# Performance work log

Hardware: AMD Instinct MI355X
Metric: run time of the kernel (lower is better)

## Reference

```python
import jax, jax.numpy as jnp
import numpy as np
from jax.scipy.special import logsumexp

NEG = -1e30  # stand-in for -inf that is safe under fp32 and vjp
MAX_SEG_LEN = 64
WITH_TRANSITION = True


def setup_inputs() -> dict:
    key = jax.random.key(0)
    k1, k2 = jax.random.split(key)
    B, S, L = 8, 512, 32
    segment_score = jax.random.normal(k1, (B, S, S, L), dtype=jnp.float32)
    transitions = jax.random.uniform(k2, (L, L), dtype=jnp.float32)  # matches nn.init.uniform_(0,1)
    return {"segment_score": segment_score, "transitions": transitions}


def _compute_log_z(segment_score, transitions, max_seg_len=MAX_SEG_LEN, with_transition=WITH_TRANSITION):
    # segment_score: [B, S, S, L] (start, end, label); transitions: [L, L]
    B, S, _, L = segment_score.shape
    M = max_seg_len
    dt = segment_score.dtype
    diag = jnp.diagonal(transitions)  # [L]

    # alpha_pad slot (p + M) holds log_alpha at frame p; slots < M act as -inf guard
    alpha_pad = jnp.full((B, S + M, L), NEG, dtype=dt)
    alpha_pad = alpha_pad.at[:, M, :].set(segment_score[:, 0, 0, :])

    w = jnp.arange(M)
    j = (M - w).astype(dt)  # window slot w corresponds to segment length j = M - w
    # transition term for a continuation segment of length j ending in label cur, coming from prev:
    # T[prev, cur] + diag[cur] * (j - 1)   -> [M, prev, cur]
    trans_term = transitions[None, :, :] + diag[None, None, :] * (j[:, None, None] - 1.0)

    def step(alpha_pad, f_end):
        # segment scores for all segments ending at f_end: [B, S, L]
        seg_col = jax.lax.dynamic_index_in_dim(segment_score, f_end, axis=2, keepdims=False)
        # pad so window slot w maps to start position f_end - M + 1 + w (length j = M - w)
        seg_pad = jnp.pad(seg_col, ((0, 0), (M - 1, 0), (0, 0)))
        seg_win = jax.lax.dynamic_slice_in_dim(seg_pad, f_end, M, axis=1)     # [B, M, L]
        # alpha window slot w -> frame f_end - M + w = f_end - j (guarded by NEG padding)
        alpha_win = jax.lax.dynamic_slice_in_dim(alpha_pad, f_end, M, axis=1)  # [B, M, L]

        # continuation scores: alpha[prev] + seg * j (+ transition)  -> [B, M, prev, cur]
        scores = alpha_win[:, :, :, None] + (seg_win * j[None, :, None])[:, :, None, :]
        if with_transition:
            scores = scores + trans_term[None, :, :, :]

        # initial segment [0, f_end] (no predecessor), only valid while f_end + 1 <= M
        f = f_end.astype(dt)
        init = seg_col[:, 0, :] * (f + 1.0)
        if with_transition:
            init = init + diag[None, :] * f
        init = jnp.where(f_end < M, init, NEG)

        all_scores = jnp.concatenate([scores.reshape(B, M * L, L), init[:, None, :]], axis=1)
        new_alpha = logsumexp(all_scores, axis=1)  # [B, L]

        alpha_pad = jax.lax.dynamic_update_slice_in_dim(
            alpha_pad, new_alpha[:, None, :], f_end + M, axis=1)
        return alpha_pad, None

    alpha_pad, _ = jax.lax.scan(step, alpha_pad, jnp.arange(1, S))
    log_z = logsumexp(alpha_pad[:, S - 1 + M, :], axis=1)  # [B]
    return log_z


def reference(segment_score, transitions):
    return _compute_log_z(segment_score, transitions)
```

## Files before the change

kernel.cpp:

```cpp
#include <hip/hip_runtime.h>

#define NEGF (-1e30f)

constexpr int S = 512;
constexpr int L = 32;


template <int CTRL>
__device__ __forceinline__ float dppf(float x) {
    return __builtin_bit_cast(float,
        __builtin_amdgcn_update_dpp(0, __builtin_bit_cast(int, x),
                                    CTRL, 0xf, 0xf, true));
}
#define GR8_MAX(v) do { v = fmaxf(v, dppf<0xB1>(v));    \
                        v = fmaxf(v, dppf<0x4E>(v));    \
                        v = fmaxf(v, dppf<0x141>(v)); } while (0)
#define GR8_ADD(v) do { v += dppf<0xB1>(v);                                 \
                        v += dppf<0x4E>(v);                                 \
                        v += dppf<0x141>(v); } while (0)

#define LDS_BARRIER() do {                                                  \
    __builtin_amdgcn_fence(__ATOMIC_RELEASE, "workgroup", "local");         \
    __builtin_amdgcn_s_barrier();                                           \
    __builtin_amdgcn_fence(__ATOMIC_ACQUIRE, "workgroup", "local");         \
} while (0)

#define PREFETCH(dst, fe_) do {                                             \
    int fe2 = (fe_); if (fe2 > S - 1) fe2 = S - 1;                          \
    _Pragma("unroll")                                                       \
    for (int i = 0; i < 8; ++i) {                                           \
        const int j0 = jg * 8 + i + 1;                                      \
        int st = fe2 - j0 + 1; st = st < 0 ? 0 : st;                        \
        dst[i] = segB[((size_t)st * S + fe2) * L];                          \
    }                                                                       \
} while (0)

#define PHASE2(p_) do {                                                     \
    const int p_v = (p_);                                                   \
    const float4 a4 = *(const float4*)&alpha[p_v & 1][jg * 4];              \
    float mx = fmaxf(fmaxf(a4.x, a4.y), fmaxf(a4.z, a4.w));                 \
    GR8_MAX(mx);                                                            \
    float sb = __expf(a4.x - mx) * E0 + __expf(a4.y - mx) * E1              \
             + __expf(a4.z - mx) * E2 + __expf(a4.w - mx) * E3;             \
    GR8_ADD(sb);                                                            \
    if (jg == 0) ring[(p_v & 63) * 33 + cur] = mx + __logf(sb);             \
} while (0)

#define STEP(fe_, sv, EARLY) do {                                           \
    const int fe_v = (fe_);                                                 \
    float term[8];                                                          \
    _Pragma("unroll")                                                       \
    for (int i = 0; i < 8; ++i) {                                           \
        const int j0 = jg * 8 + i + 1;                                      \
        const float base = fmaf(sv[i], (float)j0, diag_c * (float)(j0 - 1));\
        float tv;                                                           \
        if (EARLY) {                                                        \
            tv = NEGF;                                                      \
            if (j0 <= fe_v)          tv = ring[((fe_v - j0) & 63) * 33 + cur] + base; \
            else if (j0 == fe_v + 1) tv = base;                             \
        } else {                                                            \
            tv = ring[((fe_v - j0) & 63) * 33 + cur] + base;                \
        }                                                                   \
        term[i] = tv;                                                       \
    }                                                                       \
    float M = fmaxf(fmaxf(fmaxf(term[0], term[1]), fmaxf(term[2], term[3])),\
                    fmaxf(fmaxf(term[4], term[5]), fmaxf(term[6], term[7])));\
    GR8_MAX(M);                                                             \
    float ss = ((__expf(term[0] - M) + __expf(term[1] - M)) +               \
                (__expf(term[2] - M) + __expf(term[3] - M))) +              \
               ((__expf(term[4] - M) + __expf(term[5] - M)) +               \
                (__expf(term[6] - M) + __expf(term[7] - M)));               \
    GR8_ADD(ss);                                                            \
    if (jg == 0) alpha[fe_v & 1][cur] = M + __logf(ss);                     \
    LDS_BARRIER();                                                          \
    PHASE2(fe_v);                                                           \
} while (0)

__launch_bounds__(256, 1)
__global__ void semicrf_fwd(const float* __restrict__ seg,
                            const float* __restrict__ trans,
                            float* __restrict__ out)
{
    const int t   = threadIdx.x;
    const int b   = blockIdx.x;
    const int cur = t >> 3;
    const int jg  = t & 7;

    __shared__ float ring[64 * 33];
    __shared__ float alpha[2][32];

    const float diag_c = trans[cur * 33];
    const float E0 = __expf(trans[(jg * 4 + 0) * 32 + cur]);
    const float E1 = __expf(trans[(jg * 4 + 1) * 32 + cur]);
    const float E2 = __expf(trans[(jg * 4 + 2) * 32 + cur]);
    const float E3 = __expf(trans[(jg * 4 + 3) * 32 + cur]);

    if (t < 32)
        alpha[0][t] = seg[(size_t)b * S * S * L + t];
    __syncthreads();
    PHASE2(0);

    const float* segB = seg + (size_t)b * S * S * L + cur;

    float sv0[8], sv1[8], sv2[8], sv3[8];
    PREFETCH(sv0, 1);
    PREFETCH(sv1, 2);

    for (int fe = 1; fe <= 61; fe += 4) {
        PREFETCH(sv2, fe + 2); STEP(fe + 0, sv0, true);
        PREFETCH(sv3, fe + 3); STEP(fe + 1, sv1, true);
        PREFETCH(sv0, fe + 4); STEP(fe + 2, sv2, true);
        PREFETCH(sv1, fe + 5); STEP(fe + 3, sv3, true);
    }
    for (int fe = 65; fe <= 505; fe += 4) {
        PREFETCH(sv2, fe + 2); STEP(fe + 0, sv0, false);
        PREFETCH(sv3, fe + 3); STEP(fe + 1, sv1, false);
        PREFETCH(sv0, fe + 4); STEP(fe + 2, sv2, false);
        PREFETCH(sv1, fe + 5); STEP(fe + 3, sv3, false);
    }
    PREFETCH(sv2, 511);
    STEP(509, sv0, false);
    STEP(510, sv1, false);
    STEP(511, sv2, false);

    if (t < 64) {
        float v  = (t < 32) ? alpha[1][t] : NEGF;
        float m  = v;
        float ss = 1.f;
        #pragma unroll
        for (int mk = 1; mk <= 32; mk <<= 1) {
            const float m2 = __shfl_xor(m, mk);
            const float s2 = __shfl_xor(ss, mk);
            const float mn = fmaxf(m, m2);
            ss = ss * __expf(m - mn) + s2 * __expf(m2 - mn);
            m  = mn;
        }
        if (t == 0) out[b] = m + __logf(ss);
    }
}

extern "C" void kernel_launch(void* const* d_in, const int* in_sizes, int n_in,
                              void* d_out, int out_size, void* d_ws, size_t ws_size,
                              hipStream_t stream) {
    const float* seg   = (const float*)d_in[0];
    const float* trans = (const float*)d_in[1];
    float* out = (float*)d_out;
    hipLaunchKernelGGL(semicrf_fwd, dim3(8), dim3(256), 0, stream,
                       seg, trans, out);
}
```

Before: 695.1 us.

## Split each step into lead j=1 term and lagged partial logsumexp to cut critical path

Restructures the recurrence so that the partial logsumexp over segment lengths j>=2 is computed one step ahead, off the critical path. The serial dependency then only needs the j=1 term combined with a precomputed (max,sum) pair. Alpha is passed as (max,sum) pairs instead of log values, which removes a log from each step. Per-step work on the dependency chain shrinks, in exchange for more complex indexing, extra state registers and a sentinel row in the ring buffer.

```diff
diff --git a/kernel.cpp b/kernel.cpp
--- a/kernel.cpp
+++ b/kernel.cpp
@@ -25,56 +25,83 @@
     __builtin_amdgcn_fence(__ATOMIC_ACQUIRE, "workgroup", "local");         \
 } while (0)
 
-#define PREFETCH(dst, fe_) do {                                             \
-    int fe2 = (fe_); if (fe2 > S - 1) fe2 = S - 1;                          \
+#define PF_LAG(dst, f_) do {                                                \
+    int fe2 = (f_); if (fe2 > S - 1) fe2 = S - 1;                           \
     _Pragma("unroll")                                                       \
     for (int i = 0; i < 8; ++i) {                                           \
-        const int j0 = jg * 8 + i + 1;                                      \
+        const int j0 = jg * 8 + i + 2;                                      \
         int st = fe2 - j0 + 1; st = st < 0 ? 0 : st;                        \
         dst[i] = segB[((size_t)st * S + fe2) * L];                          \
     }                                                                       \
 } while (0)
 
-#define PHASE2(p_) do {                                                     \
-    const int p_v = (p_);                                                   \
-    const float4 a4 = *(const float4*)&alpha[p_v & 1][jg * 4];              \
-    float mx = fmaxf(fmaxf(a4.x, a4.y), fmaxf(a4.z, a4.w));                 \
-    GR8_MAX(mx);                                                            \
-    float sb = __expf(a4.x - mx) * E0 + __expf(a4.y - mx) * E1              \
-             + __expf(a4.z - mx) * E2 + __expf(a4.w - mx) * E3;             \
-    GR8_ADD(sb);                                                            \
-    if (jg == 0) ring[(p_v & 63) * 33 + cur] = mx + __logf(sb);             \
-} while (0)
-
-#define STEP(fe_, sv, EARLY) do {                                           \
-    const int fe_v = (fe_);                                                 \
-    float term[8];                                                          \
+#define PF_S1(dst, f_) do {                                                 \
+    int fe2 = (f_); if (fe2 > S - 1) fe2 = S - 1;                           \
+    dst = segB[(size_t)fe2 * (S + 1) * L];                                  \
+} while (0)
+
+#define LAGLOAD(f_, lim_, rr) do {                                          \
+    const int f_v = (f_); const int lim_v = (lim_);                         \
     _Pragma("unroll")                                                       \
     for (int i = 0; i < 8; ++i) {                                           \
-        const int j0 = jg * 8 + i + 1;                                      \
-        const float base = fmaf(sv[i], (float)j0, diag_c * (float)(j0 - 1));\
-        float tv;                                                           \
-        if (EARLY) {                                                        \
-            tv = NEGF;                                                      \
-            if (j0 <= fe_v)          tv = ring[((fe_v - j0) & 63) * 33 + cur] + base; \
-            else if (j0 == fe_v + 1) tv = base;                             \
-        } else {                                                            \
-            tv = ring[((fe_v - j0) & 63) * 33 + cur] + base;                \
-        }                                                                   \
-        term[i] = tv;                                                       \
+        const int j0 = jg * 8 + i + 2;                                      \
+        int row = (f_v - j0) & 63;                                          \
+        if (j0 > lim_v || (i == 0 && jg == 0)) row = 64;                    \
+        rr[i] = ring[row * 33 + cur];                                       \
     }                                                                       \
-    float M = fmaxf(fmaxf(fmaxf(term[0], term[1]), fmaxf(term[2], term[3])),\
-                    fmaxf(fmaxf(term[4], term[5]), fmaxf(term[6], term[7])));\
+} while (0)
+
+#define LEAD(k_, s1v_) do {                                                 \
+    const float t1m = bm + (s1v_);                                          \
+    const float Ma  = fmaxf(pM, t1m);                                       \
+    const float Sa  = pS * __expf(pM - Ma) + __expf(t1m - Ma);              \
+    if (jg == 0) {                                                          \
+        *(float2*)&aMS[(k_)&1][cur * 2] = make_float2(Ma, Sa);              \
+        ring[(((k_) - 1) & 63) * 33 + cur] = bm;                            \
+    }                                                                       \
+} while (0)
+
+#define LAGCOMP(sv, rr) do {                                                \
+    float tt[8];                                                            \
+    _Pragma("unroll")                                                       \
+    for (int i = 0; i < 8; ++i)                                             \
+        tt[i] = rr[i] + fmaf(sv[i], jf[i], dj[i]);                          \
+    if (jg == 0) tt[0] = bm + fmaf(sv[0], jf[0], dj[0]);                    \
+    float M = fmaxf(fmaxf(fmaxf(tt[0],tt[1]), fmaxf(tt[2],tt[3])),          \
+                    fmaxf(fmaxf(tt[4],tt[5]), fmaxf(tt[6],tt[7])));         \
     GR8_MAX(M);                                                             \
-    float ss = ((__expf(term[0] - M) + __expf(term[1] - M)) +               \
-                (__expf(term[2] - M) + __expf(term[3] - M))) +              \
-               ((__expf(term[4] - M) + __expf(term[5] - M)) +               \
-                (__expf(term[6] - M) + __expf(term[7] - M)));               \
-    GR8_ADD(ss);                                                            \
-    if (jg == 0) alpha[fe_v & 1][cur] = M + __logf(ss);                     \
+    float SS = ((__expf(tt[0]-M) + __expf(tt[1]-M)) +                       \
+                (__expf(tt[2]-M) + __expf(tt[3]-M))) +                      \
+               ((__expf(tt[4]-M) + __expf(tt[5]-M)) +                       \
+                (__expf(tt[6]-M) + __expf(tt[7]-M)));                       \
+    GR8_ADD(SS);                                                            \
+    pM = M; pS = SS;                                                        \
+} while (0)
+
+#define PHASE2(k_) do {                                                     \
+    const int par = (k_) & 1;                                               \
+    const float4 A0 = *(const float4*)&aMS[par][jg * 8];                    \
+    const float4 A1 = *(const float4*)&aMS[par][jg * 8 + 4];                \
+    float mx = fmaxf(fmaxf(A0.x, A0.z), fmaxf(A1.x, A1.z));                 \
+    GR8_MAX(mx);                                                            \
+    float sb = (A0.y * E0) * __expf(A0.x - mx) +                            \
+               (A0.w * E1) * __expf(A0.z - mx) +                            \
+               (A1.y * E2) * __expf(A1.x - mx) +                            \
+               (A1.w * E3) * __expf(A1.z - mx);                             \
+    GR8_ADD(sb);                                                            \
+    bm = mx + __logf(sb);                                                   \
+} while (0)
+
+#define STEP(k_, sv, s1v_, lim_) do {                                       \
+    float rr[8];                                                            \
+    LAGLOAD((k_) + 1, lim_, rr);                                            \
+    LEAD(k_, s1v_);                                                         \
     LDS_BARRIER();                                                          \
-    PHASE2(fe_v);                                                           \
-} while (0)
+    LAGCOMP(sv, rr);                                                        \
+    PHASE2(k_);                                                             \
+} while (0)
+
+#define LIMV(kk) (((kk) + 2) < 64 ? ((kk) + 2) : 64)
 
 __launch_bounds__(256, 1)
 __global__ void semicrf_fwd(const float* __restrict__ seg,
@@ -86,8 +113,8 @@
     const int cur = t >> 3;
     const int jg  = t & 7;
 
-    __shared__ float ring[64 * 33];
-    __shared__ float alpha[2][32];
+    __shared__ float ring[65 * 33];
+    __shared__ __align__(16) float aMS[2][64];
 
     const float diag_c = trans[cur * 33];
     const float E0 = __expf(trans[(jg * 4 + 0) * 32 + cur]);
@@ -95,36 +122,67 @@
     const float E2 = __expf(trans[(jg * 4 + 2) * 32 + cur]);
     const float E3 = __expf(trans[(jg * 4 + 3) * 32 + cur]);
 
-    if (t < 32)
-        alpha[0][t] = seg[(size_t)b * S * S * L + t];
+    float jf[8], dj[8];
+    #pragma unroll
+    for (int i = 0; i < 8; ++i) {
+        const int j0 = jg * 8 + i + 2;
+        jf[i] = (float)j0;
+        dj[i] = diag_c * (float)(j0 - 1);
+    }
+
+    const float* segB = seg + (size_t)b * S * S * L + cur;
+
+    float sv0[8], sv1[8], sv2[8], sv3[8];
+    float s10, s11, s12, s13;
+    PF_LAG(sv1, 1); PF_LAG(sv2, 2); PF_LAG(sv3, 3); PF_LAG(sv0, 4);
+    PF_S1(s11, 1);  PF_S1(s12, 2);  PF_S1(s13, 3);  PF_S1(s10, 4);
+
+    if (t < 32) {
+        ring[63 * 33 + t] = 0.0f;
+        ring[64 * 33 + t] = NEGF;
+    }
+    if (jg == 0) {
+        const float a0 = segB[0];
+        *(float2*)&aMS[0][cur * 2] = make_float2(a0, 1.0f);
+    }
     __syncthreads();
-    PHASE2(0);
-
-    const float* segB = seg + (size_t)b * S * S * L + cur;
-
-    float sv0[8], sv1[8], sv2[8], sv3[8];
-    PREFETCH(sv0, 1);
-    PREFETCH(sv1, 2);
-
-    for (int fe = 1; fe <= 61; fe += 4) {
-        PREFETCH(sv2, fe + 2); STEP(fe + 0, sv0, true);
-        PREFETCH(sv3, fe + 3); STEP(fe + 1, sv1, true);
-        PREFETCH(sv0, fe + 4); STEP(fe + 2, sv2, true);
-        PREFETCH(sv1, fe + 5); STEP(fe + 3, sv3, true);
-    }
-    for (int fe = 65; fe <= 505; fe += 4) {
-        PREFETCH(sv2, fe + 2); STEP(fe + 0, sv0, false);
-        PREFETCH(sv3, fe + 3); STEP(fe + 1, sv1, false);
-        PREFETCH(sv0, fe + 4); STEP(fe + 2, sv2, false);
-        PREFETCH(sv1, fe + 5); STEP(fe + 3, sv3, false);
-    }
-    PREFETCH(sv2, 511);
-    STEP(509, sv0, false);
-    STEP(510, sv1, false);
-    STEP(511, sv2, false);
+
+    float pM = NEGF, pS = 0.0f, bm = 0.0f;
+
+    {
+        float rr[8];
+        LAGLOAD(1, 2, rr);
+        LDS_BARRIER();
+        LAGCOMP(sv1, rr);
+        PHASE2(0);
+    }
+    PF_LAG(sv1, 5);
+
+    for (int k = 1; k <= 61; k += 4) {
+        STEP(k + 0, sv2, s11, LIMV(k + 0)); PF_LAG(sv2, k + 5); PF_S1(s11, k + 4);
+        STEP(k + 1, sv3, s12, LIMV(k + 1)); PF_LAG(sv3, k + 6); PF_S1(s12, k + 5);
+        STEP(k + 2, sv0, s13, LIMV(k + 2)); PF_LAG(sv0, k + 7); PF_S1(s13, k + 6);
+        STEP(k + 3, sv1, s10, LIMV(k + 3)); PF_LAG(sv1, k + 8); PF_S1(s10, k + 7);
+    }
+    for (int k = 65; k <= 505; k += 4) {
+        STEP(k + 0, sv2, s11, 64); PF_LAG(sv2, k + 5); PF_S1(s11, k + 4);
+        STEP(k + 1, sv3, s12, 64); PF_LAG(sv3, k + 6); PF_S1(s12, k + 5);
+        STEP(k + 2, sv0, s13, 64); PF_LAG(sv0, k + 7); PF_S1(s13, k + 6);
+        STEP(k + 3, sv1, s10, 64); PF_LAG(sv1, k + 8); PF_S1(s10, k + 7);
+    }
+    STEP(509, sv2, s11, 64);
+    STEP(510, sv3, s12, 64);
+
+    {
+        const float t1m = bm + s13;
+        const float Ma  = fmaxf(pM, t1m);
+        const float Sa  = pS * __expf(pM - Ma) + __expf(t1m - Ma);
+        if (jg == 0) *(float2*)&aMS[1][cur * 2] = make_float2(Ma, Sa);
+    }
+    __syncthreads();
 
     if (t < 64) {
-        float v  = (t < 32) ? alpha[1][t] : NEGF;
+        float v  = (t < 32) ? (aMS[1][t * 2] + __logf(aMS[1][t * 2 + 1])) : NEGF;
         float m  = v;
         float ss = 1.f;
         #pragma unroll
```

Measured after the change: 664.9 us. 1.05x faster.

## Split semi-CRF recurrence into critical-chain wave and lagged partial-sum waves

Applied to the files above, without the earlier changes.

Restructures the sequential forward pass. One wavefront now computes only the latency-critical short-lag terms (lengths 1-3) plus the transition matmul. Three other wavefronts precompute logsumexp partials for segment lengths 4-64 a few frames ahead and hand them over through LDS, synchronising with spin-wait counters instead of block-wide barriers. The aim is to shorten the per-frame critical path and remove the s_barrier each frame. In exchange the code relies on volatile-counter producer/consumer ordering, which carries correctness and deadlock risk.

```diff
diff --git a/kernel.cpp b/kernel.cpp
--- a/kernel.cpp
+++ b/kernel.cpp
@@ -12,130 +12,225 @@
         __builtin_amdgcn_update_dpp(0, __builtin_bit_cast(int, x),
                                     CTRL, 0xf, 0xf, true));
 }
-#define GR8_MAX(v) do { v = fmaxf(v, dppf<0xB1>(v));    \
-                        v = fmaxf(v, dppf<0x4E>(v));    \
-                        v = fmaxf(v, dppf<0x141>(v)); } while (0)
-#define GR8_ADD(v) do { v += dppf<0xB1>(v);                                 \
-                        v += dppf<0x4E>(v);                                 \
-                        v += dppf<0x141>(v); } while (0)
-
-#define LDS_BARRIER() do {                                                  \
-    __builtin_amdgcn_fence(__ATOMIC_RELEASE, "workgroup", "local");         \
-    __builtin_amdgcn_s_barrier();                                           \
+#define RED32_MAX(v) do { v = fmaxf(v, dppf<0xB1>(v));                      \
+                          v = fmaxf(v, dppf<0x4E>(v));                      \
+                          v = fmaxf(v, dppf<0x141>(v));                     \
+                          v = fmaxf(v, dppf<0x140>(v));                     \
+                          v = fmaxf(v, __shfl_xor(v, 16)); } while (0)
+#define RED32_ADD(v) do { v += dppf<0xB1>(v); v += dppf<0x4E>(v);           \
+                          v += dppf<0x141>(v); v += dppf<0x140>(v);         \
+                          v += __shfl_xor(v, 16); } while (0)
+
+template<int JLO, int NT0, int NT1, int W>
+__device__ __forceinline__ void lag_run(const float* __restrict__ segB,
+                                        const float* __restrict__ trans,
+                                        float* ring,
+                                        float (*part)[3][32][2],
+                                        volatile int* cnt,
+                                        int c, int h, bool lane0)
+{
+    const float diag_c = trans[c * 33];
+    const int nt = h ? NT1 : NT0;
+    const int jb = JLO + (h ? NT0 : 0);
+    float jfv[11], djv[11];
+    int idxA[11], idxB[11];
+#pragma unroll
+    for (int i = 0; i < 11; ++i) {
+        const int jj = (i < nt) ? (jb + i) : jb;
+        jfv[i] = (float)jj;
+        djv[i] = diag_c * (float)(jj - 1);
+        idxA[i] = (3 * (S + 1) - (jj - 1) * S) * L + c;
+        idxB[i] = idxA[i] + (S + 1) * L;
+    }
+    float svA[11], svB[11];
+    int cd = -1;
+
+#define LAG_PF(sv, idx, fq, MSK) do {                                       \
+    _Pragma("unroll")                                                       \
+    for (int i = 0; i < 11; ++i) {                                          \
+        int e = idx[i];                                                     \
+        if (MSK) {                                                          \
+            const bool vld = (i < nt) && (jb + i <= (fq) + 1);              \
+            e = vld ? e : ((fq) * L + c);      \
+        }                                                                   \
+        sv[i] = segB[e];                                                    \
+        idx[i] += 2 * (S + 1) * L;           \
+    }                                                                       \
+} while (0)
+
+#define LAG_FRAME(f_, sv, MSK) do {                                         \
+    const int ff = (f_);                                                    \
+    if (cd < ff - 4) {                                                      \
+        do { __builtin_amdgcn_s_sleep(1); cd = cnt[3]; } while (cd < ff - 4); \
+    }                                                                       \
     __builtin_amdgcn_fence(__ATOMIC_ACQUIRE, "workgroup", "local");         \
+    const int fj = ff - jb;                                                 \
+    float tt[11];                                                           \
+    _Pragma("unroll")                                                       \
+    for (int i = 0; i < 11; ++i) {                                          \
+        const float rv = ring[((fj - i) & 63) * 33 + c];                    \
+        const float tv = rv + fmaf(sv[i], jfv[i], djv[i]);                  \
+        bool vld = (i < nt);                                                \
+        if (MSK) vld = vld && (jb + i <= ff + 1);                           \
+        tt[i] = vld ? tv : NEGF;                                            \
+    }                                                                       \
+    float m = fmaxf(fmaxf(fmaxf(fmaxf(tt[0], tt[1]), fmaxf(tt[2], tt[3])),  \
+                          fmaxf(fmaxf(tt[4], tt[5]), fmaxf(tt[6], tt[7]))), \
+                    fmaxf(fmaxf(tt[8], tt[9]), tt[10]));                    \
+    float s = ((__expf(tt[0] - m) + __expf(tt[1] - m)) +                    \
+               (__expf(tt[2] - m) + __expf(tt[3] - m))) +                   \
+              ((__expf(tt[4] - m) + __expf(tt[5] - m)) +                    \
+               (__expf(tt[6] - m) + __expf(tt[7] - m))) +                   \
+              ((__expf(tt[8] - m) + __expf(tt[9] - m)) +                    \
+               __expf(tt[10] - m));                                         \
+    const float m2 = __shfl_xor(m, 32);                                     \
+    const float s2 = __shfl_xor(s, 32);                                     \
+    const float Mw = fmaxf(m, m2);                                          \
+    const float Sw = s * __expf(m - Mw) + s2 * __expf(m2 - Mw);             \
+    if (h == 0) *(float2*)&part[ff & 3][W][c][0] = make_float2(Mw, Sw);     \
+    asm volatile("s_waitcnt lgkmcnt(0)" ::: "memory");                      \
+    if (lane0) cnt[W] = ff;                                                 \
 } while (0)
 
-#define PREFETCH(dst, fe_) do {                                             \
-    int fe2 = (fe_); if (fe2 > S - 1) fe2 = S - 1;                          \
-    _Pragma("unroll")                                                       \
-    for (int i = 0; i < 8; ++i) {                                           \
-        const int j0 = jg * 8 + i + 1;                                      \
-        int st = fe2 - j0 + 1; st = st < 0 ? 0 : st;                        \
-        dst[i] = segB[((size_t)st * S + fe2) * L];                          \
-    }                                                                       \
-} while (0)
-
-#define PHASE2(p_) do {                                                     \
-    const int p_v = (p_);                                                   \
-    const float4 a4 = *(const float4*)&alpha[p_v & 1][jg * 4];              \
-    float mx = fmaxf(fmaxf(a4.x, a4.y), fmaxf(a4.z, a4.w));                 \
-    GR8_MAX(mx);                                                            \
-    float sb = __expf(a4.x - mx) * E0 + __expf(a4.y - mx) * E1              \
-             + __expf(a4.z - mx) * E2 + __expf(a4.w - mx) * E3;             \
-    GR8_ADD(sb);                                                            \
-    if (jg == 0) ring[(p_v & 63) * 33 + cur] = mx + __logf(sb);             \
-} while (0)
-
-#define STEP(fe_, sv, EARLY) do {                                           \
-    const int fe_v = (fe_);                                                 \
-    float term[8];                                                          \
-    _Pragma("unroll")                                                       \
-    for (int i = 0; i < 8; ++i) {                                           \
-        const int j0 = jg * 8 + i + 1;                                      \
-        const float base = fmaf(sv[i], (float)j0, diag_c * (float)(j0 - 1));\
-        float tv;                                                           \
-        if (EARLY) {                                                        \
-            tv = NEGF;                                                      \
-            if (j0 <= fe_v)          tv = ring[((fe_v - j0) & 63) * 33 + cur] + base; \
-            else if (j0 == fe_v + 1) tv = base;                             \
-        } else {                                                            \
-            tv = ring[((fe_v - j0) & 63) * 33 + cur] + base;                \
-        }                                                                   \
-        term[i] = tv;                                                       \
-    }                                                                       \
-    float M = fmaxf(fmaxf(fmaxf(term[0], term[1]), fmaxf(term[2], term[3])),\
-                    fmaxf(fmaxf(term[4], term[5]), fmaxf(term[6], term[7])));\
-    GR8_MAX(M);                                                             \
-    float ss = ((__expf(term[0] - M) + __expf(term[1] - M)) +               \
-                (__expf(term[2] - M) + __expf(term[3] - M))) +              \
-               ((__expf(term[4] - M) + __expf(term[5] - M)) +               \
-                (__expf(term[6] - M) + __expf(term[7] - M)));               \
-    GR8_ADD(ss);                                                            \
-    if (jg == 0) alpha[fe_v & 1][cur] = M + __logf(ss);                     \
-    LDS_BARRIER();                                                          \
-    PHASE2(fe_v);                                                           \
-} while (0)
+    LAG_PF(svA, idxA, 3, true);
+    LAG_PF(svB, idxB, 4, true);
+    for (int f = 3; f <= 61; f += 2) {
+        LAG_FRAME(f, svA, true);      LAG_PF(svA, idxA, f + 2, true);
+        LAG_FRAME(f + 1, svB, true);  LAG_PF(svB, idxB, f + 3, true);
+    }
+    for (int f = 63; f <= 507; f += 2) {
+        LAG_FRAME(f, svA, false);     LAG_PF(svA, idxA, f + 2, false);
+        LAG_FRAME(f + 1, svB, false); LAG_PF(svB, idxB, f + 3, false);
+    }
+    LAG_FRAME(509, svA, false);
+    LAG_PF(svA, idxA, 511, false);
+    LAG_FRAME(510, svB, false);
+    LAG_FRAME(511, svA, false);
+#undef LAG_PF
+#undef LAG_FRAME
+}
 
 __launch_bounds__(256, 1)
 __global__ void semicrf_fwd(const float* __restrict__ seg,
                             const float* __restrict__ trans,
                             float* __restrict__ out)
 {
-    const int t   = threadIdx.x;
-    const int b   = blockIdx.x;
-    const int cur = t >> 3;
-    const int jg  = t & 7;
+    const int t  = threadIdx.x;
+    const int b  = blockIdx.x;
+    const int c  = t & 31;
+    const int h  = (t >> 5) & 1;
+    const int wv = t >> 6;
 
     __shared__ float ring[64 * 33];
-    __shared__ float alpha[2][32];
-
-    const float diag_c = trans[cur * 33];
-    const float E0 = __expf(trans[(jg * 4 + 0) * 32 + cur]);
-    const float E1 = __expf(trans[(jg * 4 + 1) * 32 + cur]);
-    const float E2 = __expf(trans[(jg * 4 + 2) * 32 + cur]);
-    const float E3 = __expf(trans[(jg * 4 + 3) * 32 + cur]);
-
-    if (t < 32)
-        alpha[0][t] = seg[(size_t)b * S * S * L + t];
+    __shared__ __align__(16) float part[4][3][32][2];
+    __shared__ __align__(16) float ubuf[32];
+    __shared__ int cnt_s[4];
+
+    for (int i = t; i < 4 * 3 * 32; i += 256)
+        ((float2*)part)[i] = make_float2(NEGF, 0.f);
+    if (t < 32) ring[63 * 33 + t] = 0.f;
+    if (t < 3)  cnt_s[t] = 2;
+    if (t == 3) cnt_s[3] = -1;
     __syncthreads();
-    PHASE2(0);
-
-    const float* segB = seg + (size_t)b * S * S * L + cur;
-
-    float sv0[8], sv1[8], sv2[8], sv3[8];
-    PREFETCH(sv0, 1);
-    PREFETCH(sv1, 2);
-
-    for (int fe = 1; fe <= 61; fe += 4) {
-        PREFETCH(sv2, fe + 2); STEP(fe + 0, sv0, true);
-        PREFETCH(sv3, fe + 3); STEP(fe + 1, sv1, true);
-        PREFETCH(sv0, fe + 4); STEP(fe + 2, sv2, true);
-        PREFETCH(sv1, fe + 5); STEP(fe + 3, sv3, true);
-    }
-    for (int fe = 65; fe <= 505; fe += 4) {
-        PREFETCH(sv2, fe + 2); STEP(fe + 0, sv0, false);
-        PREFETCH(sv3, fe + 3); STEP(fe + 1, sv1, false);
-        PREFETCH(sv0, fe + 4); STEP(fe + 2, sv2, false);
-        PREFETCH(sv1, fe + 5); STEP(fe + 3, sv3, false);
-    }
-    PREFETCH(sv2, 511);
-    STEP(509, sv0, false);
-    STEP(510, sv1, false);
-    STEP(511, sv2, false);
-
-    if (t < 64) {
-        float v  = (t < 32) ? alpha[1][t] : NEGF;
-        float m  = v;
-        float ss = 1.f;
-        #pragma unroll
-        for (int mk = 1; mk <= 32; mk <<= 1) {
-            const float m2 = __shfl_xor(m, mk);
-            const float s2 = __shfl_xor(ss, mk);
-            const float mn = fmaxf(m, m2);
-            ss = ss * __expf(m - mn) + s2 * __expf(m2 - mn);
-            m  = mn;
+
+    const float* segB  = seg + (size_t)b * S * S * L;
+    volatile int* cnt  = cnt_s;
+
+    if (wv == 0) {
+        __builtin_amdgcn_s_setprio(1);
+        float E[16];
+#pragma unroll
+        for (int i = 0; i < 16; ++i)
+            E[i] = __expf(trans[(h * 16 + i) * 32 + c]);
+        const float diag_c = trans[c * 33];
+
+        float s1s[4], s2s[4], s3s[4];
+#pragma unroll
+        for (int ff = 1; ff <= 4; ++ff) {
+            const int st1 = ff, st2 = ff - 1, st3 = (ff - 2 < 0) ? 0 : ff - 2;
+            s1s[ff & 3] = segB[(st1 * S + ff) * L + c];
+            s2s[ff & 3] = segB[(st2 * S + ff) * L + c];
+            s3s[ff & 3] = segB[(st3 * S + ff) * L + c];
         }
-        if (t == 0) out[b] = m + __logf(ss);
+
+        float Ma = segB[c];
+        float Sa = 1.f;
+        float bm1 = 0.f;
+        float bm2 = NEGF;
+        int lmin = 2, l0 = 2, l1 = 2, l2 = 2;
+
+#define CHAIN_FRAME(f_, Q_) do {                                            \
+    const int ff = (f_);                                                    \
+    if (lmin < ff + 1) {                                                    \
+        do { l0 = cnt[0]; l1 = cnt[1]; l2 = cnt[2];                         \
+             lmin = min(min(l0, l1), l2); } while (lmin < ff + 1);          \
+    }                                                                       \
+    __builtin_amdgcn_fence(__ATOMIC_ACQUIRE, "workgroup", "local");         \
+                                         \
+    float mx = Ma;                                                          \
+    RED32_MAX(mx);                                                          \
+    const float uu = Sa * __expf(Ma - mx);                                  \
+    if (h == 0) ubuf[c] = uu;                                               \
+    if (t == 0) cnt[3] = ff - 1;    \
+    asm volatile("s_waitcnt lgkmcnt(0)" ::: "memory");                      \
+    const float4 uA = *(const float4*)&ubuf[h * 16 + 0];                    \
+    const float4 uB = *(const float4*)&ubuf[h * 16 + 4];                    \
+    const float4 uC = *(const float4*)&ubuf[h * 16 + 8];                    \
+    const float4 uD = *(const float4*)&ubuf[h * 16 + 12];                   \
+    const float2 P0 = *(const float2*)&part[Q_][0][c][0];                   \
+    const float2 P1 = *(const float2*)&part[Q_][1][c][0];                   \
+    const float2 P2 = *(const float2*)&part[Q_][2][c][0];                   \
+    l0 = cnt[0]; l1 = cnt[1]; l2 = cnt[2];                                  \
+    float dA = fmaf(uA.x, E[0],  fmaf(uA.y, E[1],  fmaf(uA.z, E[2],  uA.w * E[3])));  \
+    float dB = fmaf(uB.x, E[4],  fmaf(uB.y, E[5],  fmaf(uB.z, E[6],  uB.w * E[7])));  \
+    float dC = fmaf(uC.x, E[8],  fmaf(uC.y, E[9],  fmaf(uC.z, E[10], uC.w * E[11]))); \
+    float dD = fmaf(uD.x, E[12], fmaf(uD.y, E[13], fmaf(uD.z, E[14], uD.w * E[15]))); \
+    float dot = (dA + dB) + (dC + dD);                                      \
+    dot += __shfl_xor(dot, 32);                                             \
+    const float bb = mx + __logf(dot);                                      \
+    if (h == 0) ring[(ff & 63) * 33 + c] = bb;                              \
+                    \
+    const float t2v = fmaf(2.f, s2s[Q_], bm1 + diag_c);                     \
+    const float t3v = fmaf(3.f, s3s[Q_], bm2 + 2.f * diag_c);               \
+    const float Mp  = fmaxf(fmaxf(P0.x, P1.x), fmaxf(P2.x, fmaxf(t2v, t3v)));        \
+    const float Sp  = P0.y * __expf(P0.x - Mp) + P1.y * __expf(P1.x - Mp)            \
+                    + P2.y * __expf(P2.x - Mp)                              \
+                    + __expf(t2v - Mp) + __expf(t3v - Mp);                  \
+    const float t1v = bb + s1s[Q_];                                         \
+    Ma = fmaxf(Mp, t1v);                                                    \
+    Sa = fmaf(Sp, __expf(Mp - Ma), __expf(t1v - Ma));                       \
+    bm2 = bm1; bm1 = bb;                                                    \
+    lmin = min(min(l0, l1), l2);                                            \
+    { int fq = ff + 5; if (fq > 511) fq = 511;                              \
+      const int bidx = fq * (S + 1) * L + c;                                \
+      s1s[Q_] = segB[bidx];                                                 \
+      s2s[Q_] = segB[bidx - S * L];                                         \
+      s3s[Q_] = segB[bidx - 2 * S * L]; }                                   \
+} while (0)
+
+        for (int fb = 0; fb < 508; fb += 4) {
+            CHAIN_FRAME(fb + 0, 1);
+            CHAIN_FRAME(fb + 1, 2);
+            CHAIN_FRAME(fb + 2, 3);
+            CHAIN_FRAME(fb + 3, 0);
+        }
+        CHAIN_FRAME(508, 1);
+        CHAIN_FRAME(509, 2);
+        CHAIN_FRAME(510, 3);
+#undef CHAIN_FRAME
+        {
+            float mx = Ma;
+            RED32_MAX(mx);
+            float uu = Sa * __expf(Ma - mx);
+            RED32_ADD(uu);
+            if (t == 0) out[b] = mx + __logf(uu);
+        }
+    } else if (wv == 1) {
+        lag_run<4, 11, 10, 0>(segB, trans, ring, part, cnt, c, h, (t & 63) == 0);
+    } else if (wv == 2) {
+        lag_run<25, 10, 10, 1>(segB, trans, ring, part, cnt, c, h, (t & 63) == 0);
+    } else {
+        lag_run<45, 10, 10, 2>(segB, trans, ring, part, cnt, c, h, (t & 63) == 0);
     }
 }
 
```

New measurement: 789.5 us. 1.14x slower.

## Split semi-CRF recurrence into latency-critical chain wave and lagged producer waves

Applied to the files above, without the earlier changes.

The kernel is restructured into one wavefront that runs the serial recurrence with only the short-lag terms (segment lengths 1-15), plus three producer wavefronts. The producers precompute partial logsumexp contributions for the long-lag terms (lengths 16-64) several frames ahead and hand them over through LDS, synchronising with spin-polled counters instead of block barriers. The transition step becomes an exp-space dot product over a broadcast buffer. This aims to shorten the per-frame critical path and remove the workgroup barrier from every step. In exchange it adds custom spin-wait synchronisation with a capped spin count, which risks races or silent wrong results if the lag assumptions are off.

```diff
diff --git a/kernel.cpp b/kernel.cpp
--- a/kernel.cpp
+++ b/kernel.cpp
@@ -4,6 +4,13 @@
 
 constexpr int S = 512;
 constexpr int L = 32;
+constexpr int SL1 = (S + 1) * L;
+constexpr int SLN = S * L;
+constexpr int SSL = S * S * L;
+constexpr int RSTR = 33;
+constexpr int RROWS = 128;
+constexpr int RWRAP = RROWS * RSTR;
+constexpr int SPIN_CAP = 1 << 20;
 
 
 template <int CTRL>
@@ -12,68 +19,130 @@
         __builtin_amdgcn_update_dpp(0, __builtin_bit_cast(int, x),
                                     CTRL, 0xf, 0xf, true));
 }
-#define GR8_MAX(v) do { v = fmaxf(v, dppf<0xB1>(v));    \
-                        v = fmaxf(v, dppf<0x4E>(v));    \
-                        v = fmaxf(v, dppf<0x141>(v)); } while (0)
-#define GR8_ADD(v) do { v += dppf<0xB1>(v);                                 \
-                        v += dppf<0x4E>(v);                                 \
-                        v += dppf<0x141>(v); } while (0)
-
-#define LDS_BARRIER() do {                                                  \
-    __builtin_amdgcn_fence(__ATOMIC_RELEASE, "workgroup", "local");         \
-    __builtin_amdgcn_s_barrier();                                           \
-    __builtin_amdgcn_fence(__ATOMIC_ACQUIRE, "workgroup", "local");         \
+#define RED32_MAX(v) do { v = fmaxf(v, dppf<0xB1>(v));                      \
+                          v = fmaxf(v, dppf<0x4E>(v));                      \
+                          v = fmaxf(v, dppf<0x141>(v));                     \
+                          v = fmaxf(v, dppf<0x140>(v));                     \
+                          v = fmaxf(v, __shfl_xor(v, 16)); } while (0)
+
+#define CHAIN(ff_, SBUF, DOPOLL, DOPUB) do {                                \
+    const int ff = (ff_);                                                   \
+       \
+    float tj[14];                                                           \
+    _Pragma("unroll")                                                       \
+    for (int i = 0; i < 14; ++i)                                            \
+        tj[i] = bH[i] + fmaf(SBUF[i + 1], (float)(i + 2), dgc[i]);          \
+    float Mp = fmaxf(pp1.x, tj[0]);                                         \
+    _Pragma("unroll")                                                       \
+    for (int i = 1; i < 14; ++i) Mp = fmaxf(Mp, tj[i]);                     \
+    float Sp = pp1.y * __expf(pp1.x - Mp);                                  \
+    _Pragma("unroll")                                                       \
+    for (int i = 0; i < 14; ++i) Sp += __expf(tj[i] - Mp);                  \
+    float mxn = Ma;                                                         \
+    RED32_MAX(mxn);                     \
+                               \
+    const float uu = Sa * __expf(Ma - mx);                                  \
+    if (t < 32) ubuf[c] = uu;                                               \
+    const float4 u0 = *(const float4*)&ubuf[0];                             \
+    const float4 u1 = *(const float4*)&ubuf[4];                             \
+    const float4 u2 = *(const float4*)&ubuf[8];                             \
+    const float4 u3 = *(const float4*)&ubuf[12];                            \
+    const float4 u4 = *(const float4*)&ubuf[16];                            \
+    const float4 u5 = *(const float4*)&ubuf[20];                            \
+    const float4 u6 = *(const float4*)&ubuf[24];                            \
+    const float4 u7 = *(const float4*)&ubuf[28];                            \
+    float d0 = u0.x * E[0];                                                 \
+    d0 = fmaf(u0.y, E[1], d0);  d0 = fmaf(u0.z, E[2], d0);                  \
+    d0 = fmaf(u0.w, E[3], d0);  d0 = fmaf(u1.x, E[4], d0);                  \
+    d0 = fmaf(u1.y, E[5], d0);  d0 = fmaf(u1.z, E[6], d0);                  \
+    d0 = fmaf(u1.w, E[7], d0);                                              \
+    float d1 = u2.x * E[8];                                                 \
+    d1 = fmaf(u2.y, E[9],  d1); d1 = fmaf(u2.z, E[10], d1);                 \
+    d1 = fmaf(u2.w, E[11], d1); d1 = fmaf(u3.x, E[12], d1);                 \
+    d1 = fmaf(u3.y, E[13], d1); d1 = fmaf(u3.z, E[14], d1);                 \
+    d1 = fmaf(u3.w, E[15], d1);                                             \
+    float d2 = u4.x * E[16];                                                \
+    d2 = fmaf(u4.y, E[17], d2); d2 = fmaf(u4.z, E[18], d2);                 \
+    d2 = fmaf(u4.w, E[19], d2); d2 = fmaf(u5.x, E[20], d2);                 \
+    d2 = fmaf(u5.y, E[21], d2); d2 = fmaf(u5.z, E[22], d2);                 \
+    d2 = fmaf(u5.w, E[23], d2);                                             \
+    float d3 = u6.x * E[24];                                                \
+    d3 = fmaf(u6.y, E[25], d3); d3 = fmaf(u6.z, E[26], d3);                 \
+    d3 = fmaf(u6.w, E[27], d3); d3 = fmaf(u7.x, E[28], d3);                 \
+    d3 = fmaf(u7.y, E[29], d3); d3 = fmaf(u7.z, E[30], d3);                 \
+    d3 = fmaf(u7.w, E[31], d3);                                             \
+    const float dot = (d0 + d1) + (d2 + d3);                                \
+    const float bb = mx + __logf(dot);                                      \
+    if (t < 32) ring[wadr] = bb;                                            \
+    wadr += RSTR; if (wadr >= RWRAP) wadr -= RWRAP;                         \
+                                                  \
+    const float t1 = bb + SBUF[0];                                          \
+    const float Man = fmaxf(Mp, t1);                                        \
+    Sa = fmaf(Sp, __expf(Mp - Man), __expf(t1 - Man));                      \
+    Ma = Man;                                                               \
+    mx = mxn;                                                               \
+    if (DOPUB) {                                                            \
+        asm volatile("s_waitcnt lgkmcnt(0)" ::: "memory");                  \
+        if (t == 0) cntv[3] = ff;                                           \
+    }                                                                       \
+    if (DOPOLL) {                                                           \
+        const int Fb = ff + 3;                                              \
+        if (Fb <= 508) {                                                    \
+            volatile int* cw = &cntv[(Fb >> 2) % 3];                        \
+            int zz = 0;                                                     \
+            while (*cw < Fb && ++zz < SPIN_CAP) {}                          \
+            __builtin_amdgcn_fence(__ATOMIC_ACQUIRE, "workgroup", "local"); \
+        }                                                                   \
+    }                                                                       \
+    pp1 = pp2;                                                              \
+    pp2 = part[(ff + 3) & 31][c];                                           \
+    _Pragma("unroll")                                                       \
+    for (int i = 13; i > 0; --i) bH[i] = bH[i - 1];                         \
+    bH[0] = bb;                                                             \
+             \
+    _Pragma("unroll")                                                       \
+    for (int i = 0; i < 15; ++i) {                                          \
+        int o = offv[i];                                                    \
+        o = (o < (int)c || o >= SSL) ? (int)c : o;    \
+        SBUF[i] = segB[o];                                                  \
+        offv[i] += SL1;                                                     \
+    }                                                                       \
 } while (0)
 
-#define PREFETCH(dst, fe_) do {                                             \
-    int fe2 = (fe_); if (fe2 > S - 1) fe2 = S - 1;                          \
-    _Pragma("unroll")                                                       \
-    for (int i = 0; i < 8; ++i) {                                           \
-        const int j0 = jg * 8 + i + 1;                                      \
-        int st = fe2 - j0 + 1; st = st < 0 ? 0 : st;                        \
-        dst[i] = segB[((size_t)st * S + fe2) * L];                          \
+#define LLOAD(BUF) do {                                                     \
+    _Pragma("unroll")                                                       \
+    for (int i = 0; i < 25; ++i) {                                          \
+        int o = offs[i];                                                    \
+        o = (o < (int)c || o >= SSL) ? (int)c : o;                          \
+        BUF[i] = segB[o];                                                   \
+        offs[i] += SL1;                                                     \
     }                                                                       \
 } while (0)
 
-#define PHASE2(p_) do {                                                     \
-    const int p_v = (p_);                                                   \
-    const float4 a4 = *(const float4*)&alpha[p_v & 1][jg * 4];              \
-    float mx = fmaxf(fmaxf(a4.x, a4.y), fmaxf(a4.z, a4.w));                 \
-    GR8_MAX(mx);                                                            \
-    float sb = __expf(a4.x - mx) * E0 + __expf(a4.y - mx) * E1              \
-             + __expf(a4.z - mx) * E2 + __expf(a4.w - mx) * E3;             \
-    GR8_ADD(sb);                                                            \
-    if (jg == 0) ring[(p_v & 63) * 33 + cur] = mx + __logf(sb);             \
-} while (0)
-
-#define STEP(fe_, sv, EARLY) do {                                           \
-    const int fe_v = (fe_);                                                 \
-    float term[8];                                                          \
-    _Pragma("unroll")                                                       \
-    for (int i = 0; i < 8; ++i) {                                           \
-        const int j0 = jg * 8 + i + 1;                                      \
-        const float base = fmaf(sv[i], (float)j0, diag_c * (float)(j0 - 1));\
-        float tv;                                                           \
-        if (EARLY) {                                                        \
-            tv = NEGF;                                                      \
-            if (j0 <= fe_v)          tv = ring[((fe_v - j0) & 63) * 33 + cur] + base; \
-            else if (j0 == fe_v + 1) tv = base;                             \
-        } else {                                                            \
-            tv = ring[((fe_v - j0) & 63) * 33 + cur] + base;                \
-        }                                                                   \
-        term[i] = tv;                                                       \
-    }                                                                       \
-    float M = fmaxf(fmaxf(fmaxf(term[0], term[1]), fmaxf(term[2], term[3])),\
-                    fmaxf(fmaxf(term[4], term[5]), fmaxf(term[6], term[7])));\
-    GR8_MAX(M);                                                             \
-    float ss = ((__expf(term[0] - M) + __expf(term[1] - M)) +               \
-                (__expf(term[2] - M) + __expf(term[3] - M))) +              \
-               ((__expf(term[4] - M) + __expf(term[5] - M)) +               \
-                (__expf(term[6] - M) + __expf(term[7] - M)));               \
-    GR8_ADD(ss);                                                            \
-    if (jg == 0) alpha[fe_v & 1][cur] = M + __logf(ss);                     \
-    LDS_BARRIER();                                                          \
-    PHASE2(fe_v);                                                           \
+#define LFRAME(ff_, BUF, MSK) do {                                          \
+    const int ff = (ff_);                                                   \
+    float tt[25];                                                           \
+    _Pragma("unroll")                                                       \
+    for (int i = 0; i < 25; ++i) {                                          \
+        const float rv = ring[radr[i]];                                     \
+        const float tv = rv + fmaf(BUF[i], jfv[i], dgv[i]);                 \
+        bool vld = (i < nt);                                                \
+        if (MSK) vld = vld && (jlo + i <= ff + 1);                          \
+        tt[i] = vld ? tv : NEGF;                                            \
+        radr[i] += RSTR;                                                    \
+        if (radr[i] >= RWRAP) radr[i] -= RWRAP;                             \
+    }                                                                       \
+    float m = tt[0];                                                        \
+    _Pragma("unroll")                                                       \
+    for (int i = 1; i < 25; ++i) m = fmaxf(m, tt[i]);                       \
+    float s = 0.f;                                                          \
+    _Pragma("unroll")                                                       \
+    for (int i = 0; i < 25; ++i) s += __expf(tt[i] - m);                    \
+    const float m2 = __shfl_xor(m, 32);                                     \
+    const float s2 = __shfl_xor(s, 32);                                     \
+    const float Mw = fmaxf(m, m2);                                          \
+    const float Sw = fmaf(s, __expf(m - Mw), s2 * __expf(m2 - Mw));         \
+    if (h == 0) part[ff & 31][c] = make_float2(Mw, Sw);                     \
 } while (0)
 
 __launch_bounds__(256, 1)
@@ -81,54 +150,82 @@
                             const float* __restrict__ trans,
                             float* __restrict__ out)
 {
-    const int t   = threadIdx.x;
-    const int b   = blockIdx.x;
-    const int cur = t >> 3;
-    const int jg  = t & 7;
-
-    __shared__ float ring[64 * 33];
-    __shared__ float alpha[2][32];
-
-    const float diag_c = trans[cur * 33];
-    const float E0 = __expf(trans[(jg * 4 + 0) * 32 + cur]);
-    const float E1 = __expf(trans[(jg * 4 + 1) * 32 + cur]);
-    const float E2 = __expf(trans[(jg * 4 + 2) * 32 + cur]);
-    const float E3 = __expf(trans[(jg * 4 + 3) * 32 + cur]);
-
-    if (t < 32)
-        alpha[0][t] = seg[(size_t)b * S * S * L + t];
+    const int t  = threadIdx.x;
+    const int b  = blockIdx.x;
+    const int c  = t & 31;
+    const int h  = (t >> 5) & 1;
+    const int wv = t >> 6;
+
+    __shared__ float ring[RROWS * RSTR];
+    __shared__ float2 part[32][32];
+    __shared__ __align__(16) float ubuf[32];
+    __shared__ int cnt_s[4];
+
+    if (t < 32) ring[t] = 0.f;
+    if (t < 4)  cnt_s[t] = -1;
     __syncthreads();
-    PHASE2(0);
-
-    const float* segB = seg + (size_t)b * S * S * L + cur;
-
-    float sv0[8], sv1[8], sv2[8], sv3[8];
-    PREFETCH(sv0, 1);
-    PREFETCH(sv1, 2);
-
-    for (int fe = 1; fe <= 61; fe += 4) {
-        PREFETCH(sv2, fe + 2); STEP(fe + 0, sv0, true);
-        PREFETCH(sv3, fe + 3); STEP(fe + 1, sv1, true);
-        PREFETCH(sv0, fe + 4); STEP(fe + 2, sv2, true);
-        PREFETCH(sv1, fe + 5); STEP(fe + 3, sv3, true);
-    }
-    for (int fe = 65; fe <= 505; fe += 4) {
-        PREFETCH(sv2, fe + 2); STEP(fe + 0, sv0, false);
-        PREFETCH(sv3, fe + 3); STEP(fe + 1, sv1, false);
-        PREFETCH(sv0, fe + 4); STEP(fe + 2, sv2, false);
-        PREFETCH(sv1, fe + 5); STEP(fe + 3, sv3, false);
-    }
-    PREFETCH(sv2, 511);
-    STEP(509, sv0, false);
-    STEP(510, sv1, false);
-    STEP(511, sv2, false);
-
-    if (t < 64) {
-        float v  = (t < 32) ? alpha[1][t] : NEGF;
-        float m  = v;
+
+    const float* segB = seg + (size_t)b * S * S * L;
+    volatile int* cntv = cnt_s;
+
+    if (wv == 0) {
+        __builtin_amdgcn_s_setprio(1);
+        float E[32];
+#pragma unroll
+        for (int i = 0; i < 32; ++i) E[i] = __expf(trans[i * 32 + c]);
+        const float diag_c = trans[c * 33];
+        float dgc[14];
+#pragma unroll
+        for (int i = 0; i < 14; ++i) dgc[i] = diag_c * (float)(i + 1);
+
+        float bH[14];
+        bH[0] = 0.f;
+#pragma unroll
+        for (int i = 1; i < 14; ++i) bH[i] = NEGF;
+
+        float sO[15], sE[15];
+        int offv[15];
+#pragma unroll
+        for (int i = 0; i < 15; ++i) {
+            const int j = i + 1;
+            int o1 = 1 * SL1 - (j - 1) * SLN + (int)c;
+            int o2 = 2 * SL1 - (j - 1) * SLN + (int)c;
+            o1 = o1 < (int)c ? (int)c : o1;
+            o2 = o2 < (int)c ? (int)c : o2;
+            sO[i] = segB[o1];
+            sE[i] = segB[o2];
+            offv[i] = 3 * SL1 - (j - 1) * SLN + (int)c;
+        }
+
+        float Ma = segB[c];
+        float Sa = 1.f;
+        float mx = Ma;
+        RED32_MAX(mx);
+        int wadr = RSTR + (int)c;
+
+        {
+            volatile int* cw = &cntv[0];
+            int zz = 0;
+            while (*cw < 0 && ++zz < SPIN_CAP) {}
+            __builtin_amdgcn_fence(__ATOMIC_ACQUIRE, "workgroup", "local");
+        }
+        float2 pp1 = part[1][c];
+        float2 pp2 = part[2][c];
+
+        for (int f = 0; f < 508; f += 4) {
+            CHAIN(f + 0, sO, false, false);
+            CHAIN(f + 1, sE, true,  false);
+            CHAIN(f + 2, sO, false, false);
+            CHAIN(f + 3, sE, false, true);
+        }
+        CHAIN(508, sO, false, false);
+        CHAIN(509, sE, true,  false);
+        CHAIN(510, sO, false, false);
+
+        float m = Ma + __logf(Sa);
         float ss = 1.f;
-        #pragma unroll
-        for (int mk = 1; mk <= 32; mk <<= 1) {
+#pragma unroll
+        for (int mk = 1; mk <= 16; mk <<= 1) {
             const float m2 = __shfl_xor(m, mk);
             const float s2 = __shfl_xor(ss, mk);
             const float mn = fmaxf(m, m2);
@@ -136,6 +233,62 @@
             m  = mn;
         }
         if (t == 0) out[b] = m + __logf(ss);
+    } else {
+        const int wl  = wv - 1;
+        const int jlo = h ? 41 : 16;
+        const int nt  = h ? 24 : 25;
+        const float diag_c = trans[c * 33];
+
+        float jfv[25], dgv[25];
+        int offs[25], radr[25];
+        const int F0 = 4 * wl;
+#pragma unroll
+        for (int i = 0; i < 25; ++i) {
+            const int j = jlo + i;
+            jfv[i] = (float)j;
+            dgv[i] = diag_c * (float)(j - 1);
+            offs[i] = F0 * SL1 - (j - 1) * SLN + (int)c;
+            const int row = (F0 - j + 1) & (RROWS - 1);
+            radr[i] = row * RSTR + (int)c;
+        }
+
+        float bufA[25], bufB[25];
+        int cdv = -1;
+        int F = F0;
+        LLOAD(bufA);
+        LLOAD(bufB);
+        while (F <= 508) {
+            if (F >= 16) {
+                const int need = F - 13;
+                int zz = 0;
+                while (cdv < need && ++zz < SPIN_CAP) {
+                    __builtin_amdgcn_s_sleep(1); cdv = cntv[3];
+                }
+                __builtin_amdgcn_fence(__ATOMIC_ACQUIRE, "workgroup", "local");
+            }
+            if (F <= 60) {
+                LFRAME(F + 0, bufA, true);  LLOAD(bufA);
+                LFRAME(F + 1, bufB, true);  LLOAD(bufB);
+                LFRAME(F + 2, bufA, true);
+                LFRAME(F + 3, bufB, true);
+            } else {
+                LFRAME(F + 0, bufA, false); LLOAD(bufA);
+                LFRAME(F + 1, bufB, false); LLOAD(bufB);
+                LFRAME(F + 2, bufA, false);
+                LFRAME(F + 3, bufB, false);
+            }
+            asm volatile("s_waitcnt lgkmcnt(0)" ::: "memory");
+            if ((t & 63) == 0) cntv[wl] = F;
+#pragma unroll
+            for (int i = 0; i < 25; ++i) offs[i] += 8 * SL1;
+#pragma unroll
+            for (int i = 0; i < 25; ++i) {
+                radr[i] += 8 * RSTR;
+                if (radr[i] >= RWRAP) radr[i] -= RWRAP;
+            }
+            F += 12;
+            if (F <= 508) { LLOAD(bufA); LLOAD(bufB); }
+        }
     }
 }
 
```

Result: faster. 646.2 us (-7.0%).
